# Optimization experiments

Hardware: AMD Instinct MI355X
Metric: run time of the kernel (lower is better)

## Reference

```python
import jax, jax.numpy as jnp
import numpy as np

B = 8192          # batch size
D = 128           # embedding_dim
R = 1000          # relation_dict_len
MARGIN = 1.0


def setup_inputs() -> dict:
    key = jax.random.key(0)
    k1, k2, k3, k4 = jax.random.split(key, 4)
    return {
        "positive_batch": jax.random.normal(k1, (B, 3, D), dtype=jnp.float32),
        "negative_batch": jax.random.normal(k2, (B, 3, D), dtype=jnp.float32),
        "r_idx": jax.random.randint(k3, (B,), 0, R),
        "rel_emb": jax.random.normal(k4, (R, D * D), dtype=jnp.float32),
    }


def _score(batch, Wr):
    # batch: (B, 3, D) -> h, r, t each (B, D); Wr: (B, D, D)
    h, r, t = batch[:, 0], batch[:, 1], batch[:, 2]
    d = jnp.abs(h + r - t)                       # (B, D)
    # x^T Wr x quadratic form per example, fused in one einsum
    return jnp.einsum('bi,bij,bj->b', d, Wr, d)  # (B,)


def reference(positive_batch, negative_batch, r_idx, rel_emb):
    # Gather per-example relation matrix (Wr built from positive relation,
    # reused for the negative score, as in the original module).
    Wr = rel_emb[r_idx].reshape(-1, D, D)        # (B, D, D)
    pos = _score(positive_batch, Wr)
    neg = _score(negative_batch, Wr)
    return jnp.mean(jax.nn.relu(MARGIN + pos - neg))
```

## Files before the change

### kernel.cpp

```cpp
#include <hip/hip_runtime.h>

#define BATCH 8192
#define DIM 128
#define NREL 1000
#define MARGIN 1.0f
#define GRID 1400
#define ORDER_CAP 11264

#define WS_PA 0
#define WS_PB 8192
#define WS_ORDER 16384

__global__ __launch_bounds__(1024) void sort_kernel(const int* __restrict__ r_idx,
                                                    int* __restrict__ order) {
  __shared__ int s_cnt[1024];
  __shared__ int s_cur[1024];
  __shared__ int s_wsum[16];
  const int tid = threadIdx.x, lane = tid & 63, wave = tid >> 6;
  s_cnt[tid] = 0;
  __syncthreads();
  int my[8];
#pragma unroll
  for (int k = 0; k < 8; ++k) {
    my[k] = r_idx[tid + k * 1024];
    atomicAdd(&s_cnt[my[k]], 1);
  }
  __syncthreads();
  const int c = (s_cnt[tid] + 3) & ~3;
  int v = c;
#pragma unroll
  for (int o = 1; o < 64; o <<= 1) {
    int u = __shfl_up(v, o, 64);
    if (lane >= o) v += u;
  }
  if (lane == 63) s_wsum[wave] = v;
  __syncthreads();
  int woff = 0;
  for (int w = 0; w < wave; ++w) woff += s_wsum[w];
  s_cur[tid] = woff + v - c;
  for (int i = tid; i < ORDER_CAP; i += 1024) order[i] = -1;
  __syncthreads();
#pragma unroll
  for (int k = 0; k < 8; ++k) {
    int p = atomicAdd(&s_cur[my[k]], 1);
    order[p] = tid + k * 1024;
  }
}

__device__ inline float2 dvec(const float* __restrict__ b, int c0) {
  float2 h = *(const float2*)(b + c0);
  float2 r = *(const float2*)(b + DIM + c0);
  float2 t = *(const float2*)(b + 2 * DIM + c0);
  return make_float2(fabsf(h.x + r.x - t.x), fabsf(h.y + r.y - t.y));
}

__global__ __launch_bounds__(256) void score_kernel(
    const float* __restrict__ pos_b, const float* __restrict__ neg_b,
    const int* __restrict__ r_idx, const float* __restrict__ rel_emb,
    const int* __restrict__ order, float* __restrict__ pA,
    float* __restrict__ pB) {
  __shared__ float s_d[4][64 * 20];
  const int tid = threadIdx.x, lane = tid & 63, wave = tid >> 6;
  const int phys = blockIdx.x;
  const int lb = (phys & 7) * (GRID / 8) + (phys >> 3);
  const int pair = wave >> 1, half = wave & 1;
  const int g = lb * 2 + pair;
  int4 es = *(const int4*)(order + g * 4);
  if (es.x < 0) return;

  const int c0 = lane * 2;
  const int r = r_idx[es.x];
  const bool v1 = es.y >= 0, v2 = es.z >= 0, v3 = es.w >= 0;
  const int e1 = v1 ? es.y : es.x, e2 = v2 ? es.z : es.x, e3 = v3 ? es.w : es.x;

  const float2 z = make_float2(0.f, 0.f);
  float2 dp0 = dvec(pos_b + (size_t)es.x * 3 * DIM, c0);
  float2 dn0 = dvec(neg_b + (size_t)es.x * 3 * DIM, c0);
  float2 dp1 = v1 ? dvec(pos_b + (size_t)e1 * 3 * DIM, c0) : z;
  float2 dn1 = v1 ? dvec(neg_b + (size_t)e1 * 3 * DIM, c0) : z;
  float2 dp2 = v2 ? dvec(pos_b + (size_t)e2 * 3 * DIM, c0) : z;
  float2 dn2 = v2 ? dvec(neg_b + (size_t)e2 * 3 * DIM, c0) : z;
  float2 dp3 = v3 ? dvec(pos_b + (size_t)e3 * 3 * DIM, c0) : z;
  float2 dn3 = v3 ? dvec(neg_b + (size_t)e3 * 3 * DIM, c0) : z;

  {
    float* myd = &s_d[wave][lane * 20];
    *(float4*)(myd + 0)  = make_float4(dp0.x, dp1.x, dp2.x, dp3.x);
    *(float4*)(myd + 4)  = make_float4(dn0.x, dn1.x, dn2.x, dn3.x);
    *(float4*)(myd + 8)  = make_float4(dp0.y, dp1.y, dp2.y, dp3.y);
    *(float4*)(myd + 12) = make_float4(dn0.y, dn1.y, dn2.y, dn3.y);
  }

  const int colb = (lane & 31) * 4;
  const int rsel = lane >> 5;
  const float* W = rel_emb + (size_t)r * (DIM * DIM) +
                   (size_t)(half * 64 + rsel) * DIM + colb;
  const float* dptr = &s_d[wave][(half * 32) * 20 + rsel * 8];

  const float4 fz = make_float4(0.f, 0.f, 0.f, 0.f);
  float4 ap0 = fz, ap1 = fz, ap2 = fz, ap3 = fz;
  float4 an0 = fz, an1 = fz, an2 = fz, an3 = fz;

#define FMA4(ACC, D, WV)          \
  ACC.x = fmaf(D, WV.x, ACC.x);   \
  ACC.y = fmaf(D, WV.y, ACC.y);   \
  ACC.z = fmaf(D, WV.z, ACC.z);   \
  ACC.w = fmaf(D, WV.w, ACC.w);

#pragma unroll 8
  for (int it = 0; it < 32; ++it) {
    float4 wv = *(const float4*)(W + (size_t)(it * 2) * DIM);
    float4 ddp = *(const float4*)(dptr + it * 20);
    float4 ddn = *(const float4*)(dptr + it * 20 + 4);
    FMA4(ap0, ddp.x, wv) FMA4(ap1, ddp.y, wv)
    FMA4(ap2, ddp.z, wv) FMA4(ap3, ddp.w, wv)
    FMA4(an0, ddn.x, wv) FMA4(an1, ddn.y, wv)
    FMA4(an2, ddn.z, wv) FMA4(an3, ddn.w, wv)
  }
#undef FMA4

  const int sl0 = (lane & 31) * 2, sl1 = sl0 + 1;
#define GET4(OUT0, OUT1, OUT2, OUT3, V)   \
  OUT0 = __shfl(V.x, sl0, 64);            \
  OUT1 = __shfl(V.y, sl0, 64);            \
  OUT2 = __shfl(V.x, sl1, 64);            \
  OUT3 = __shfl(V.y, sl1, 64);
  float a, b, c, d, e, f, gg, h;
  float s0, s1, s2, s3;
  GET4(a, b, c, d, dp0) GET4(e, f, gg, h, dn0)
  s0 = ap0.x * a + ap0.y * b + ap0.z * c + ap0.w * d -
       (an0.x * e + an0.y * f + an0.z * gg + an0.w * h);
  GET4(a, b, c, d, dp1) GET4(e, f, gg, h, dn1)
  s1 = ap1.x * a + ap1.y * b + ap1.z * c + ap1.w * d -
       (an1.x * e + an1.y * f + an1.z * gg + an1.w * h);
  GET4(a, b, c, d, dp2) GET4(e, f, gg, h, dn2)
  s2 = ap2.x * a + ap2.y * b + ap2.z * c + ap2.w * d -
       (an2.x * e + an2.y * f + an2.z * gg + an2.w * h);
  GET4(a, b, c, d, dp3) GET4(e, f, gg, h, dn3)
  s3 = ap3.x * a + ap3.y * b + ap3.z * c + ap3.w * d -
       (an3.x * e + an3.y * f + an3.z * gg + an3.w * h);
#undef GET4

#pragma unroll
  for (int o = 32; o > 0; o >>= 1) {
    s0 += __shfl_xor(s0, o, 64);
    s1 += __shfl_xor(s1, o, 64);
    s2 += __shfl_xor(s2, o, 64);
    s3 += __shfl_xor(s3, o, 64);
  }
  float* P = half ? pB : pA;
  if (lane == 0) {
    P[es.x] = s0;
    if (v1) P[es.y] = s1;
    if (v2) P[es.z] = s2;
    if (v3) P[es.w] = s3;
  }
}

__global__ __launch_bounds__(256) void reduce_kernel(const float* __restrict__ pA,
                                                     const float* __restrict__ pB,
                                                     float* __restrict__ out) {
  float acc = 0.f;
  for (int i = threadIdx.x; i < BATCH; i += 256) {
    float v = MARGIN + pA[i] + pB[i];
    acc += (v > 0.f) ? v : 0.f;
  }
#pragma unroll
  for (int o = 32; o > 0; o >>= 1) acc += __shfl_xor(acc, o, 64);
  __shared__ float s[4];
  const int lane = threadIdx.x & 63, wave = threadIdx.x >> 6;
  if (lane == 0) s[wave] = acc;
  __syncthreads();
  if (threadIdx.x == 0) out[0] = (s[0] + s[1] + s[2] + s[3]) * (1.0f / BATCH);
}

extern "C" void kernel_launch(void* const* d_in, const int* in_sizes, int n_in,
                              void* d_out, int out_size, void* d_ws, size_t ws_size,
                              hipStream_t stream) {
  const float* pos_b = (const float*)d_in[0];
  const float* neg_b = (const float*)d_in[1];
  const int* r_idx = (const int*)d_in[2];
  const float* rel_emb = (const float*)d_in[3];
  float* out = (float*)d_out;

  float* pA = (float*)d_ws + WS_PA;
  float* pB = (float*)d_ws + WS_PB;
  int* order = (int*)d_ws + WS_ORDER;

  sort_kernel<<<1, 1024, 0, stream>>>(r_idx, order);
  score_kernel<<<GRID, 256, 0, stream>>>(pos_b, neg_b, r_idx, rel_emb, order,
                                         pA, pB);
  reduce_kernel<<<1, 256, 0, stream>>>(pA, pB, out);
}
```

Before: 43.97 us.

## Split sort into multi-block hist/scan/scatter and give each block one group

Replaces the single-block counting sort with three kernels: a global-atomic histogram, a single-block scan and a multi-block scatter, plus memsets to clear the counters and the order buffer. The score kernel now gives each 256-thread block one 4-example group, with the four waves each covering a quarter of the Wr rows. Partials are combined through shared memory, which removes the separate pA/pB buffers. The aim is to cut the serial single-block sort and raise parallelism per group, at the cost of more launches, global atomics and an extra block barrier.

```diff
diff --git a/kernel.cpp b/kernel.cpp
--- a/kernel.cpp
+++ b/kernel.cpp
@@ -4,47 +4,54 @@
 #define DIM 128
 #define NREL 1000
 #define MARGIN 1.0f
-#define GRID 1400
-#define ORDER_CAP 11264
-
-#define WS_PA 0
-#define WS_PB 8192
-#define WS_ORDER 16384
-
-__global__ __launch_bounds__(1024) void sort_kernel(const int* __restrict__ r_idx,
-                                                    int* __restrict__ order) {
-  __shared__ int s_cnt[1024];
-  __shared__ int s_cur[1024];
-  __shared__ int s_wsum[16];
+#define GRID 2800
+#define ORDER_CAP 11200
+
+#define WS_PARTIAL 0
+#define WS_CNT 8192
+#define WS_ORDER 9216
+
+__global__ __launch_bounds__(256) void hist_kernel(const int* __restrict__ r_idx,
+                                                   int* __restrict__ cnt) {
+  const int i = blockIdx.x * 256 + threadIdx.x;
+  atomicAdd(&cnt[r_idx[i]], 1);
+}
+
+__global__ __launch_bounds__(256) void scan_kernel(int* __restrict__ cnt) {
   const int tid = threadIdx.x, lane = tid & 63, wave = tid >> 6;
-  s_cnt[tid] = 0;
-  __syncthreads();
-  int my[8];
-#pragma unroll
-  for (int k = 0; k < 8; ++k) {
-    my[k] = r_idx[tid + k * 1024];
-    atomicAdd(&s_cnt[my[k]], 1);
-  }
-  __syncthreads();
-  const int c = (s_cnt[tid] + 3) & ~3;
-  int v = c;
+  const int base = tid * 4;
+  int c[4], lsum = 0;
+#pragma unroll
+  for (int k = 0; k < 4; ++k) {
+    const int i = base + k;
+    c[k] = (i < NREL) ? ((cnt[i] + 3) & ~3) : 0;
+    lsum += c[k];
+  }
+  int v = lsum;
 #pragma unroll
   for (int o = 1; o < 64; o <<= 1) {
     int u = __shfl_up(v, o, 64);
     if (lane >= o) v += u;
   }
-  if (lane == 63) s_wsum[wave] = v;
+  __shared__ int wsum[4];
+  if (lane == 63) wsum[wave] = v;
   __syncthreads();
   int woff = 0;
-  for (int w = 0; w < wave; ++w) woff += s_wsum[w];
-  s_cur[tid] = woff + v - c;
-  for (int i = tid; i < ORDER_CAP; i += 1024) order[i] = -1;
-  __syncthreads();
-#pragma unroll
-  for (int k = 0; k < 8; ++k) {
-    int p = atomicAdd(&s_cur[my[k]], 1);
-    order[p] = tid + k * 1024;
-  }
+  for (int w = 0; w < wave; ++w) woff += wsum[w];
+  int toff = woff + v - lsum;
+#pragma unroll
+  for (int k = 0; k < 4; ++k) {
+    cnt[base + k] = toff;
+    toff += c[k];
+  }
+}
+
+__global__ __launch_bounds__(256) void scatter_kernel(const int* __restrict__ r_idx,
+                                                      int* __restrict__ cursor,
+                                                      int* __restrict__ order) {
+  const int i = blockIdx.x * 256 + threadIdx.x;
+  const int p = atomicAdd(&cursor[r_idx[i]], 1);
+  order[p] = i;
 }
 
 __device__ inline float2 dvec(const float* __restrict__ b, int c0) {
@@ -57,14 +64,12 @@
 __global__ __launch_bounds__(256) void score_kernel(
     const float* __restrict__ pos_b, const float* __restrict__ neg_b,
     const int* __restrict__ r_idx, const float* __restrict__ rel_emb,
-    const int* __restrict__ order, float* __restrict__ pA,
-    float* __restrict__ pB) {
-  __shared__ float s_d[4][64 * 20];
+    const int* __restrict__ order, float* __restrict__ partial) {
+  __shared__ float s_d[64 * 20];
+  __shared__ float s_ps[4][4];
   const int tid = threadIdx.x, lane = tid & 63, wave = tid >> 6;
   const int phys = blockIdx.x;
-  const int lb = (phys & 7) * (GRID / 8) + (phys >> 3);
-  const int pair = wave >> 1, half = wave & 1;
-  const int g = lb * 2 + pair;
+  const int g = (phys & 7) * (GRID / 8) + (phys >> 3);
   int4 es = *(const int4*)(order + g * 4);
   if (es.x < 0) return;
 
@@ -83,19 +88,20 @@
   float2 dp3 = v3 ? dvec(pos_b + (size_t)e3 * 3 * DIM, c0) : z;
   float2 dn3 = v3 ? dvec(neg_b + (size_t)e3 * 3 * DIM, c0) : z;
 
-  {
-    float* myd = &s_d[wave][lane * 20];
+  if (wave == 0) {
+    float* myd = &s_d[lane * 20];
     *(float4*)(myd + 0)  = make_float4(dp0.x, dp1.x, dp2.x, dp3.x);
     *(float4*)(myd + 4)  = make_float4(dn0.x, dn1.x, dn2.x, dn3.x);
     *(float4*)(myd + 8)  = make_float4(dp0.y, dp1.y, dp2.y, dp3.y);
     *(float4*)(myd + 12) = make_float4(dn0.y, dn1.y, dn2.y, dn3.y);
   }
+  __syncthreads();
 
   const int colb = (lane & 31) * 4;
   const int rsel = lane >> 5;
   const float* W = rel_emb + (size_t)r * (DIM * DIM) +
-                   (size_t)(half * 64 + rsel) * DIM + colb;
-  const float* dptr = &s_d[wave][(half * 32) * 20 + rsel * 8];
+                   (size_t)(wave * 32 + rsel) * DIM + colb;
+  const float* dptr = s_d + (wave * 16) * 20 + rsel * 8;
 
   const float4 fz = make_float4(0.f, 0.f, 0.f, 0.f);
   float4 ap0 = fz, ap1 = fz, ap2 = fz, ap3 = fz;
@@ -108,7 +114,7 @@
   ACC.w = fmaf(D, WV.w, ACC.w);
 
 #pragma unroll 8
-  for (int it = 0; it < 32; ++it) {
+  for (int it = 0; it < 16; ++it) {
     float4 wv = *(const float4*)(W + (size_t)(it * 2) * DIM);
     float4 ddp = *(const float4*)(dptr + it * 20);
     float4 ddn = *(const float4*)(dptr + it * 20 + 4);
@@ -148,30 +154,41 @@
     s2 += __shfl_xor(s2, o, 64);
     s3 += __shfl_xor(s3, o, 64);
   }
-  float* P = half ? pB : pA;
   if (lane == 0) {
-    P[es.x] = s0;
-    if (v1) P[es.y] = s1;
-    if (v2) P[es.z] = s2;
-    if (v3) P[es.w] = s3;
-  }
-}
-
-__global__ __launch_bounds__(256) void reduce_kernel(const float* __restrict__ pA,
-                                                     const float* __restrict__ pB,
-                                                     float* __restrict__ out) {
+    s_ps[wave][0] = s0; s_ps[wave][1] = s1;
+    s_ps[wave][2] = s2; s_ps[wave][3] = s3;
+  }
+  __syncthreads();
+  if (tid == 0) {
+    float t0 = s_ps[0][0] + s_ps[1][0] + s_ps[2][0] + s_ps[3][0];
+    float t1 = s_ps[0][1] + s_ps[1][1] + s_ps[2][1] + s_ps[3][1];
+    float t2 = s_ps[0][2] + s_ps[1][2] + s_ps[2][2] + s_ps[3][2];
+    float t3 = s_ps[0][3] + s_ps[1][3] + s_ps[2][3] + s_ps[3][3];
+    partial[es.x] = t0;
+    if (v1) partial[es.y] = t1;
+    if (v2) partial[es.z] = t2;
+    if (v3) partial[es.w] = t3;
+  }
+}
+
+__global__ __launch_bounds__(1024) void reduce_kernel(const float* __restrict__ partial,
+                                                      float* __restrict__ out) {
   float acc = 0.f;
-  for (int i = threadIdx.x; i < BATCH; i += 256) {
-    float v = MARGIN + pA[i] + pB[i];
+  for (int i = threadIdx.x; i < BATCH; i += 1024) {
+    float v = MARGIN + partial[i];
     acc += (v > 0.f) ? v : 0.f;
   }
 #pragma unroll
   for (int o = 32; o > 0; o >>= 1) acc += __shfl_xor(acc, o, 64);
-  __shared__ float s[4];
+  __shared__ float s[16];
   const int lane = threadIdx.x & 63, wave = threadIdx.x >> 6;
   if (lane == 0) s[wave] = acc;
   __syncthreads();
-  if (threadIdx.x == 0) out[0] = (s[0] + s[1] + s[2] + s[3]) * (1.0f / BATCH);
+  if (threadIdx.x == 0) {
+    float t = 0.f;
+    for (int w = 0; w < 16; ++w) t += s[w];
+    out[0] = t * (1.0f / BATCH);
+  }
 }
 
 extern "C" void kernel_launch(void* const* d_in, const int* in_sizes, int n_in,
@@ -183,12 +200,16 @@
   const float* rel_emb = (const float*)d_in[3];
   float* out = (float*)d_out;
 
-  float* pA = (float*)d_ws + WS_PA;
-  float* pB = (float*)d_ws + WS_PB;
+  float* partial = (float*)d_ws + WS_PARTIAL;
+  int* cnt = (int*)d_ws + WS_CNT;
   int* order = (int*)d_ws + WS_ORDER;
 
-  sort_kernel<<<1, 1024, 0, stream>>>(r_idx, order);
+  hipMemsetAsync(cnt, 0, 1024 * sizeof(int), stream);
+  hipMemsetAsync(order, 0xFF, ORDER_CAP * sizeof(int), stream);
+  hist_kernel<<<BATCH / 256, 256, 0, stream>>>(r_idx, cnt);
+  scan_kernel<<<1, 256, 0, stream>>>(cnt);
+  scatter_kernel<<<BATCH / 256, 256, 0, stream>>>(r_idx, cnt, order);
   score_kernel<<<GRID, 256, 0, stream>>>(pos_b, neg_b, r_idx, rel_emb, order,
-                                         pA, pB);
-  reduce_kernel<<<1, 256, 0, stream>>>(pA, pB, out);
-}
+                                         partial);
+  reduce_kernel<<<1, 1024, 0, stream>>>(partial, out);
+}
```

Result: slower. 46.66 us (+6.1%).

## Split each block's matrix rows across four waves for one example group

Applied to the files above, without the earlier changes.

Each block now processes a single group of four same-relation examples rather than two groups. The four waves each handle a quarter of the relation matrix rows, so every thread runs 16 iterations instead of 32. The grid doubles to cover all groups, and four per-example partial sums go into a float4 workspace that the reduce kernel sums. The aim is more waves in flight to hide the latency of gathering relation matrices, at the cost of each wave redundantly loading the triple vectors for its group.

```diff
diff --git a/kernel.cpp b/kernel.cpp
--- a/kernel.cpp
+++ b/kernel.cpp
@@ -4,12 +4,11 @@
 #define DIM 128
 #define NREL 1000
 #define MARGIN 1.0f
-#define GRID 1400
+#define GRID 2816
 #define ORDER_CAP 11264
 
-#define WS_PA 0
-#define WS_PB 8192
-#define WS_ORDER 16384
+#define WS_PARTIAL 0
+#define WS_ORDER 32768
 
 __global__ __launch_bounds__(1024) void sort_kernel(const int* __restrict__ r_idx,
                                                     int* __restrict__ order) {
@@ -57,14 +56,11 @@
 __global__ __launch_bounds__(256) void score_kernel(
     const float* __restrict__ pos_b, const float* __restrict__ neg_b,
     const int* __restrict__ r_idx, const float* __restrict__ rel_emb,
-    const int* __restrict__ order, float* __restrict__ pA,
-    float* __restrict__ pB) {
+    const int* __restrict__ order, float* __restrict__ partial4) {
   __shared__ float s_d[4][64 * 20];
   const int tid = threadIdx.x, lane = tid & 63, wave = tid >> 6;
   const int phys = blockIdx.x;
-  const int lb = (phys & 7) * (GRID / 8) + (phys >> 3);
-  const int pair = wave >> 1, half = wave & 1;
-  const int g = lb * 2 + pair;
+  const int g = (phys & 7) * (GRID / 8) + (phys >> 3);
   int4 es = *(const int4*)(order + g * 4);
   if (es.x < 0) return;
 
@@ -91,11 +87,11 @@
     *(float4*)(myd + 12) = make_float4(dn0.y, dn1.y, dn2.y, dn3.y);
   }
 
-  const int colb = (lane & 31) * 4;
-  const int rsel = lane >> 5;
+  const int lam = lane & 31, rsel = lane >> 5;
+  const int colb = lam * 4;
   const float* W = rel_emb + (size_t)r * (DIM * DIM) +
-                   (size_t)(half * 64 + rsel) * DIM + colb;
-  const float* dptr = &s_d[wave][(half * 32) * 20 + rsel * 8];
+                   (size_t)(wave * 32 + rsel) * DIM + colb;
+  const float* dbase = &s_d[wave][(wave * 16) * 20 + rsel * 8];
 
   const float4 fz = make_float4(0.f, 0.f, 0.f, 0.f);
   float4 ap0 = fz, ap1 = fz, ap2 = fz, ap3 = fz;
@@ -107,11 +103,11 @@
   ACC.z = fmaf(D, WV.z, ACC.z);   \
   ACC.w = fmaf(D, WV.w, ACC.w);
 
-#pragma unroll 8
-  for (int it = 0; it < 32; ++it) {
+#pragma unroll 16
+  for (int it = 0; it < 16; ++it) {
     float4 wv = *(const float4*)(W + (size_t)(it * 2) * DIM);
-    float4 ddp = *(const float4*)(dptr + it * 20);
-    float4 ddn = *(const float4*)(dptr + it * 20 + 4);
+    float4 ddp = *(const float4*)(dbase + it * 20);
+    float4 ddn = *(const float4*)(dbase + it * 20 + 4);
     FMA4(ap0, ddp.x, wv) FMA4(ap1, ddp.y, wv)
     FMA4(ap2, ddp.z, wv) FMA4(ap3, ddp.w, wv)
     FMA4(an0, ddn.x, wv) FMA4(an1, ddn.y, wv)
@@ -119,7 +115,7 @@
   }
 #undef FMA4
 
-  const int sl0 = (lane & 31) * 2, sl1 = sl0 + 1;
+  const int sl0 = lam * 2, sl1 = sl0 + 1;
 #define GET4(OUT0, OUT1, OUT2, OUT3, V)   \
   OUT0 = __shfl(V.x, sl0, 64);            \
   OUT1 = __shfl(V.y, sl0, 64);            \
@@ -148,21 +144,20 @@
     s2 += __shfl_xor(s2, o, 64);
     s3 += __shfl_xor(s3, o, 64);
   }
-  float* P = half ? pB : pA;
   if (lane == 0) {
-    P[es.x] = s0;
-    if (v1) P[es.y] = s1;
-    if (v2) P[es.z] = s2;
-    if (v3) P[es.w] = s3;
+    partial4[es.x * 4 + wave] = s0;
+    if (v1) partial4[es.y * 4 + wave] = s1;
+    if (v2) partial4[es.z * 4 + wave] = s2;
+    if (v3) partial4[es.w * 4 + wave] = s3;
   }
 }
 
-__global__ __launch_bounds__(256) void reduce_kernel(const float* __restrict__ pA,
-                                                     const float* __restrict__ pB,
+__global__ __launch_bounds__(256) void reduce_kernel(const float* __restrict__ partial4,
                                                      float* __restrict__ out) {
   float acc = 0.f;
   for (int i = threadIdx.x; i < BATCH; i += 256) {
-    float v = MARGIN + pA[i] + pB[i];
+    float4 q = *(const float4*)(partial4 + i * 4);
+    float v = MARGIN + q.x + q.y + q.z + q.w;
     acc += (v > 0.f) ? v : 0.f;
   }
 #pragma unroll
@@ -183,12 +178,11 @@
   const float* rel_emb = (const float*)d_in[3];
   float* out = (float*)d_out;
 
-  float* pA = (float*)d_ws + WS_PA;
-  float* pB = (float*)d_ws + WS_PB;
+  float* partial4 = (float*)d_ws + WS_PARTIAL;
   int* order = (int*)d_ws + WS_ORDER;
 
   sort_kernel<<<1, 1024, 0, stream>>>(r_idx, order);
   score_kernel<<<GRID, 256, 0, stream>>>(pos_b, neg_b, r_idx, rel_emb, order,
-                                         pA, pB);
-  reduce_kernel<<<1, 256, 0, stream>>>(pA, pB, out);
+                                         partial4);
+  reduce_kernel<<<1, 256, 0, stream>>>(partial4, out);
 }
```

Measured after the change: 46.17 us. 5.0% more time.
